# Optimization experiments

Measured on AMD Instinct MI355X. Metric: run time of the kernel, lower is better.

Reference implementation:

```python
import jax, jax.numpy as jnp
import numpy as np

H = 16
N_TASKS, N_DATA, N_DEV = 400_000, 200_000, 8


def _edges(key, n_src, n_dst, e):
    k1, k2 = jax.random.split(key)
    src = jax.random.randint(k1, (e,), 0, n_src)
    dst = jax.random.randint(k2, (e,), 0, n_dst)
    return jnp.stack([src, dst]).astype(jnp.int64)


def setup_inputs() -> dict:
    key = jax.random.key(0)
    ks = jax.random.split(key, 16)
    inp = {
        "x_tasks": jax.random.normal(ks[0], (N_TASKS, 12), jnp.float32),
        "x_data": jax.random.normal(ks[1], (N_DATA, 5), jnp.float32),
        "x_devices": jax.random.normal(ks[2], (N_DEV, 12), jnp.float32),
        "ei_data_tasks": _edges(ks[3], N_DATA, N_TASKS, 1_600_000),
        "ei_tasks_data": _edges(ks[4], N_TASKS, N_DATA, 1_600_000),
        "ei_tasks_devices": _edges(ks[5], N_TASKS, N_DEV, 400_000),
        "ei_devices_tasks": _edges(ks[6], N_DEV, N_TASKS, 400_000),
        "ei_data_devices": _edges(ks[7], N_DATA, N_DEV, 200_000),
        "ei_devices_data": _edges(ks[8], N_DEV, N_DATA, 200_000),
        "ei_tt_to": _edges(ks[9], N_TASKS, N_TASKS, 800_000),
        "ei_tt_from": _edges(ks[10], N_TASKS, N_TASKS, 800_000),
        # stacked GraphConv weights, grouped by input dim
        # W_rel5:  [0]=data->tasks, [1]=data->devices
        "W_rel5": jax.random.normal(ks[11], (2, 5, H), jnp.float32) * 0.3,
        # W_rel12: [0]=tasks->data,[1]=tasks->devices,[2]=devices->tasks,[3]=devices->data,[4]=tt_to,[5]=tt_from
        "W_rel12": jax.random.normal(ks[12], (6, 12, H), jnp.float32) * 0.2,
        # b_rel order: dt_t, t_d, t_dev, dev_t, d_dev, dev_d, tt_to, tt_from
        "b_rel": jax.random.normal(ks[13], (8, H), jnp.float32) * 0.1,
        # W_root5: [0]=tasks->data (dst data), [1]=devices->data
        "W_root5": jax.random.normal(ks[14], (2, 5, H), jnp.float32) * 0.3,
        # W_root12: [0]=data->tasks,[1]=tasks->devices,[2]=devices->tasks,[3]=data->devices,[4]=tt_to,[5]=tt_from
        "W_root12": jax.random.normal(ks[15], (6, 12, H), jnp.float32) * 0.2,
        # LayerNorm params: [0]=tasks, [1]=data, [2]=devices
        "ln_gamma": jnp.ones((3, H), jnp.float32),
        "ln_beta": jnp.zeros((3, H), jnp.float32),
    }
    return inp


def _graph_conv(x_src, x_dst, ei, W_rel, b_rel, W_root):
    # PyG GraphConv(aggr='add'): lin_rel(scatter_add(x_src[src] -> dst)) + lin_root(x_dst)
    agg = jax.ops.segment_sum(x_src[ei[0]], ei[1], num_segments=x_dst.shape[0])
    return agg @ W_rel + b_rel + x_dst @ W_root


def _layer_norm(x, gamma, beta, eps=1e-5):
    mu = jnp.mean(x, axis=-1, keepdims=True)
    var = jnp.mean(jnp.square(x - mu), axis=-1, keepdims=True)
    return (x - mu) * jax.lax.rsqrt(var + eps) * gamma + beta


def reference(x_tasks, x_data, x_devices,
              ei_data_tasks, ei_tasks_data, ei_tasks_devices, ei_devices_tasks,
              ei_data_devices, ei_devices_data, ei_tt_to, ei_tt_from,
              W_rel5, W_rel12, b_rel, W_root5, W_root12, ln_gamma, ln_beta):
    # HeteroConv(aggr='sum'): sum relation outputs per destination node type
    tasks = (
        _graph_conv(x_data, x_tasks, ei_data_tasks, W_rel5[0], b_rel[0], W_root12[0])
        + _graph_conv(x_devices, x_tasks, ei_devices_tasks, W_rel12[2], b_rel[3], W_root12[2])
        + _graph_conv(x_tasks, x_tasks, ei_tt_to, W_rel12[4], b_rel[6], W_root12[4])
        + _graph_conv(x_tasks, x_tasks, ei_tt_from, W_rel12[5], b_rel[7], W_root12[5])
    )
    data = (
        _graph_conv(x_tasks, x_data, ei_tasks_data, W_rel12[0], b_rel[1], W_root5[0])
        + _graph_conv(x_devices, x_data, ei_devices_data, W_rel12[3], b_rel[5], W_root5[1])
    )
    devices = (
        _graph_conv(x_tasks, x_devices, ei_tasks_devices, W_rel12[1], b_rel[2], W_root12[1])
        + _graph_conv(x_data, x_devices, ei_data_devices, W_rel5[1], b_rel[4], W_root12[3])
    )
    slope = 0.01
    tasks = jax.nn.leaky_relu(_layer_norm(tasks, ln_gamma[0], ln_beta[0]), slope)
    data = jax.nn.leaky_relu(_layer_norm(data, ln_gamma[1], ln_beta[1]), slope)
    devices = jax.nn.leaky_relu(_layer_norm(devices, ln_gamma[2], ln_beta[2]), slope)
    return tasks, data, devices
```

## Files before the change

### kernel.cpp

```cpp
#include <hip/hip_runtime.h>
#include <hip/hip_fp16.h>

#define LRELU(v) ((v) >= 0.0f ? (v) : 0.01f * (v))
#define EPB 8192
#define SHIFT 7
#define PAIRS 1600

struct PartDesc {
    const int* src; const int* dst;
    unsigned* part; int* cursor;
    int E, B, cap, chunk0;
};

struct PrepArgs {
    PartDesc r[6];
    int part_end;
    const int *tdev_e; int E_tdev; int sd12_b0, sd12_nb;
    const int *ddev_e; int E_ddev; int sd5_b0, sd5_nb;
    const float *x_tasks, *x_data, *x_dev;
    float *aggT_dev, *aggD_dev;
    __half *h_tasks; int NT; int ct_b0;
    __half *h_data;  int ND; int cd_b0;
};

template<int F>
__device__ __forceinline__ void loadrow(const float* __restrict__ x, unsigned s, float* v) {
    const float* p = x + (size_t)s * F;
    #pragma unroll
    for (int f = 0; f < F; ++f) v[f] = p[f];
}
template<>
__device__ __forceinline__ void loadrow<12>(const float* __restrict__ x, unsigned s, float* v) {
    const float4* p = (const float4*)(x + (size_t)s * 12);
    float4 a = p[0], b = p[1], c = p[2];
    v[0]=a.x; v[1]=a.y; v[2]=a.z; v[3]=a.w;
    v[4]=b.x; v[5]=b.y; v[6]=b.z; v[7]=b.w;
    v[8]=c.x; v[9]=c.y; v[10]=c.z; v[11]=c.w;
}

template<int F>
__device__ void scatter_dev_body(const float* __restrict__ x, const int* __restrict__ src,
                                 const int* __restrict__ dst, int E,
                                 float* __restrict__ agg, float* s_agg,
                                 int bl, int nb, int t)
{
    for (int i = t; i < 8 * F; i += 256) s_agg[i] = 0.0f;
    __syncthreads();
    const int stride = nb * 256;
    for (int e = bl * 256 + t; e < E; e += stride) {
        float v[F];
        loadrow<F>(x, (unsigned)src[e], v);
        int d = dst[e];
        #pragma unroll
        for (int f = 0; f < F; ++f) atomicAdd(&s_agg[d * F + f], v[f]);
    }
    __syncthreads();
    if (t < 8 * F) atomicAdd(&agg[t], s_agg[t]);
}

__global__ __launch_bounds__(256)
void prep_k(PrepArgs A)
{
    __shared__ unsigned shp[2 * PAIRS];
    const int bid = blockIdx.x;
    const int t = threadIdx.x;

    if (bid < A.part_end) {
        unsigned* hist = shp;
        unsigned* base = shp + PAIRS;
        int ri = 0;
        #pragma unroll
        for (int k = 1; k < 6; ++k) if (bid >= A.r[k].chunk0) ri = k;
        const PartDesc d = A.r[ri];
        const int e0 = (bid - d.chunk0) * EPB;
        const int e1 = min(d.E, e0 + EPB);
        const int npair = (d.B + 1) >> 1;

        for (int i = t; i < npair; i += 256) hist[i] = 0u;
        __syncthreads();
        for (int e = e0 + t; e < e1; e += 256) {
            int b = d.dst[e] >> SHIFT;
            atomicAdd(&hist[b >> 1], 1u << ((b & 1) << 4));
        }
        __syncthreads();
        for (int i = t; i < npair; i += 256) {
            unsigned h = hist[i];
            unsigned lo = h & 0xffffu, hi = h >> 16;
            unsigned blo = lo ? (unsigned)atomicAdd(&d.cursor[2 * i],     (int)lo) : 0u;
            unsigned bhi = hi ? (unsigned)atomicAdd(&d.cursor[2 * i + 1], (int)hi) : 0u;
            base[i] = (blo & 0xffffu) | (bhi << 16);
            hist[i] = 0u;
        }
        __syncthreads();
        for (int e = e0 + t; e < e1; e += 256) {
            int dd = d.dst[e];
            int b = dd >> SHIFT;
            unsigned s16 = (unsigned)(b & 1) << 4;
            unsigned r = atomicAdd(&hist[b >> 1], 1u << s16);
            unsigned idx = ((r >> s16) & 0xffffu) + ((base[b >> 1] >> s16) & 0xffffu);
            if ((int)idx < d.cap)
                d.part[(size_t)b * d.cap + idx] =
                    ((unsigned)d.src[e] << SHIFT) | ((unsigned)dd & 127u);
        }
    } else if (bid < A.sd5_b0) {
        scatter_dev_body<12>(A.x_tasks, A.tdev_e, A.tdev_e + A.E_tdev, A.E_tdev,
                             A.aggT_dev, (float*)shp, bid - A.sd12_b0, A.sd12_nb, t);
    } else if (bid < A.ct_b0) {
        scatter_dev_body<5>(A.x_data, A.ddev_e, A.ddev_e + A.E_ddev, A.E_ddev,
                            A.aggD_dev, (float*)shp, bid - A.sd5_b0, A.sd5_nb, t);
    } else if (bid < A.cd_b0) {
        int row = (bid - A.ct_b0) * 256 + t;
        if (row < A.NT) {
            const float* xr = A.x_tasks + (size_t)row * 12;
            __half h[16];
            #pragma unroll
            for (int j = 0; j < 12; ++j) h[j] = __float2half(xr[j]);
            #pragma unroll
            for (int j = 12; j < 16; ++j) h[j] = __half(0.0f);
            uint4* dst = (uint4*)(A.h_tasks + (size_t)row * 16);
            dst[0] = *(const uint4*)h;
            dst[1] = *(const uint4*)(h + 8);
        }
    } else {
        int row = (bid - A.cd_b0) * 256 + t;
        if (row < A.ND) {
            const float* xr = A.x_data + (size_t)row * 5;
            __half h[8];
            #pragma unroll
            for (int j = 0; j < 5; ++j) h[j] = __float2half(xr[j]);
            #pragma unroll
            for (int j = 5; j < 8; ++j) h[j] = __half(0.0f);
            *(uint4*)(A.h_data + (size_t)row * 8) = *(const uint4*)h;
        }
    }
}

struct LoadH8 {
    const __half* x;
    __device__ __forceinline__ void operator()(unsigned s, float* v) const {
        uint4 u = *(const uint4*)(x + (size_t)s * 8);
        const __half2* h = (const __half2*)&u;
        float2 f0 = __half22float2(h[0]);
        float2 f1 = __half22float2(h[1]);
        float2 f2 = __half22float2(h[2]);
        v[0] = f0.x; v[1] = f0.y; v[2] = f1.x; v[3] = f1.y; v[4] = f2.x;
    }
};
struct LoadH16 {
    const __half* x;
    __device__ __forceinline__ void operator()(unsigned s, float* v) const {
        const uint4* p = (const uint4*)(x + (size_t)s * 16);
        uint4 u0 = p[0], u1 = p[1];
        const __half2* a = (const __half2*)&u0;
        const __half2* b = (const __half2*)&u1;
        float2 f;
        f = __half22float2(a[0]); v[0] = f.x; v[1] = f.y;
        f = __half22float2(a[1]); v[2] = f.x; v[3] = f.y;
        f = __half22float2(a[2]); v[4] = f.x; v[5] = f.y;
        f = __half22float2(a[3]); v[6] = f.x; v[7] = f.y;
        f = __half22float2(b[0]); v[8] = f.x; v[9] = f.y;
        f = __half22float2(b[1]); v[10] = f.x; v[11] = f.y;
    }
};
struct LoadF12 {
    const float* x;
    __device__ __forceinline__ void operator()(unsigned s, float* v) const {
        loadrow<12>(x, s, v);
    }
};

template<int F, int STR, class LD>
__device__ __forceinline__
void agg_rel(const unsigned* __restrict__ p, int cnt, LD ld, float* __restrict__ acc, int t)
{
    int i = t;
    for (; i + 256 < cnt; i += 512) {
        unsigned e0 = p[i], e1 = p[i + 256];
        float v0[F], v1[F];
        ld(e0 >> SHIFT, v0);
        ld(e1 >> SHIFT, v1);
        float* a0 = acc + (e0 & 127u) * STR;
        float* a1 = acc + (e1 & 127u) * STR;
        #pragma unroll
        for (int f = 0; f < F; ++f) atomicAdd(a0 + f, v0[f]);
        #pragma unroll
        for (int f = 0; f < F; ++f) atomicAdd(a1 + f, v1[f]);
    }
    if (i < cnt) {
        unsigned e = p[i];
        float v[F];
        ld(e >> SHIFT, v);
        float* a = acc + (e & 127u) * STR;
        #pragma unroll
        for (int f = 0; f < F; ++f) atomicAdd(a + f, v[f]);
    }
}

__device__ __forceinline__ void fma16(float* o, float fj, const float4* __restrict__ w) {
    float4 w0 = w[0], w1 = w[1], w2 = w[2], w3 = w[3];
    o[0] =fmaf(fj,w0.x,o[0]);  o[1] =fmaf(fj,w0.y,o[1]);
    o[2] =fmaf(fj,w0.z,o[2]);  o[3] =fmaf(fj,w0.w,o[3]);
    o[4] =fmaf(fj,w1.x,o[4]);  o[5] =fmaf(fj,w1.y,o[5]);
    o[6] =fmaf(fj,w1.z,o[6]);  o[7] =fmaf(fj,w1.w,o[7]);
    o[8] =fmaf(fj,w2.x,o[8]);  o[9] =fmaf(fj,w2.y,o[9]);
    o[10]=fmaf(fj,w2.z,o[10]); o[11]=fmaf(fj,w2.w,o[11]);
    o[12]=fmaf(fj,w3.x,o[12]); o[13]=fmaf(fj,w3.y,o[13]);
    o[14]=fmaf(fj,w3.z,o[14]); o[15]=fmaf(fj,w3.w,o[15]);
}

__device__ __forceinline__
void ln_store(float* o, const float* __restrict__ sg, const float* __restrict__ sbt,
              float* __restrict__ op)
{
    float mu = 0.0f;
    #pragma unroll
    for (int k = 0; k < 16; ++k) mu += o[k];
    mu *= 0.0625f;
    float var = 0.0f;
    #pragma unroll
    for (int k = 0; k < 16; ++k) { float d = o[k] - mu; var = fmaf(d, d, var); }
    var *= 0.0625f;
    const float r = rsqrtf(var + 1e-5f);
    #pragma unroll
    for (int k = 0; k < 16; ++k) {
        float v = (o[k] - mu) * r * sg[k] + sbt[k];
        o[k] = LRELU(v);
    }
    float4* q = (float4*)op;
    const float4* s = (const float4*)o;
    q[0] = s[0]; q[1] = s[1]; q[2] = s[2]; q[3] = s[3];
}

struct FusedDesc { const unsigned* part; const int* cursor; int cap; };
struct FusedArgs {
    FusedDesc rt[4];
    FusedDesc rd[2];
    const __half *h_tasks, *h_data;
    const float *x_dev, *x_tasks, *x_data;
    const float *aggT_dev, *aggD_dev;
    const float *W_rel5, *W_rel12, *b_rel, *W_root5, *W_root12, *ln_g, *ln_b;
    float *out_tasks, *out_data, *out_dev;
    int NT, ND, NDEV, Bt, Bd;
};

__global__ __launch_bounds__(256, 6)
void fused_k(FusedArgs A)
{
    __shared__ __align__(16) float lds[6144];
    const int bid = blockIdx.x;
    const int t = threadIdx.x;

    if (bid < A.Bt) {
        float* acc = lds;
        float* sW  = lds + 5248;
        float* sb  = lds + 6096;
        float* sg  = lds + 6112;
        float* sbt = lds + 6128;

        for (int i = t; i < 5248; i += 256) acc[i] = 0.0f;
        for (int i = t; i < 80; i += 256) sW[i] = A.W_rel5[i];
        for (int i = t; i < 192; i += 256) {
            sW[80  + i] = A.W_rel12[384 + i];
            sW[272 + i] = A.W_rel12[768 + i];
            sW[464 + i] = A.W_rel12[960 + i];
            sW[656 + i] = A.W_root12[i] + A.W_root12[384 + i]
                        + A.W_root12[768 + i] + A.W_root12[960 + i];
        }
        if (t < 16) {
            sb[t]  = A.b_rel[t] + A.b_rel[48 + t] + A.b_rel[96 + t] + A.b_rel[112 + t];
            sg[t]  = A.ln_g[t];
            sbt[t] = A.ln_b[t];
        }
        __syncthreads();

        const int b = bid;
        { const FusedDesc d = A.rt[0];
          agg_rel<5, 41>(d.part + (size_t)b * d.cap, min(d.cursor[b], d.cap),
                         LoadH8{A.h_data}, acc + 0, t); }
        { const FusedDesc d = A.rt[1];
          agg_rel<12, 41>(d.part + (size_t)b * d.cap, min(d.cursor[b], d.cap),
                          LoadF12{A.x_dev}, acc + 5, t); }
        { const FusedDesc d = A.rt[2];
          agg_rel<12, 41>(d.part + (size_t)b * d.cap, min(d.cursor[b], d.cap),
                          LoadH16{A.h_tasks}, acc + 17, t); }
        { const FusedDesc d = A.rt[3];
          agg_rel<12, 41>(d.part + (size_t)b * d.cap, min(d.cursor[b], d.cap),
                          LoadH16{A.h_tasks}, acc + 29, t); }
        __syncthreads();

        if (t < 128) {
            const int i = (bid << SHIFT) + t;
            if (i < A.NT) {
                const float4* xr = (const float4*)(A.x_tasks + (size_t)i * 12);
                float4 x0 = xr[0], x1 = xr[1], x2 = xr[2];
                float o[16];
                #pragma unroll
                for (int k = 0; k < 16; ++k) o[k] = sb[k];
                const float4* w4 = (const float4*)sW;
                const float* ar = acc + t * 41;
                #pragma unroll
                for (int j = 0; j < 41; ++j) fma16(o, ar[j], w4 + 4 * j);
                float xf[12] = {x0.x,x0.y,x0.z,x0.w, x1.x,x1.y,x1.z,x1.w, x2.x,x2.y,x2.z,x2.w};
                #pragma unroll
                for (int j = 0; j < 12; ++j) fma16(o, xf[j], w4 + 4 * (41 + j));
                ln_store(o, sg, sbt, A.out_tasks + (size_t)i * 16);
            }
        }
    } else if (bid < A.Bt + A.Bd) {
        float* acc = lds;
        float* sW  = lds + 3200;
        float* sb  = lds + 3664;
        float* sg  = lds + 3680;
        float* sbt = lds + 3696;

        for (int i = t; i < 3200; i += 256) acc[i] = 0.0f;
        for (int i = t; i < 192; i += 256) {
            sW[i]       = A.W_rel12[i];
            sW[192 + i] = A.W_rel12[576 + i];
        }
        for (int i = t; i < 80; i += 256)
            sW[384 + i] = A.W_root5[i] + A.W_root5[80 + i];
        if (t < 16) {
            sb[t]  = A.b_rel[16 + t] + A.b_rel[80 + t];
            sg[t]  = A.ln_g[16 + t];
            sbt[t] = A.ln_b[16 + t];
        }
        __syncthreads();

        const int b = bid - A.Bt;
        { const FusedDesc d = A.rd[0];
          agg_rel<12, 25>(d.part + (size_t)b * d.cap, min(d.cursor[b], d.cap),
                          LoadH16{A.h_tasks}, acc + 0, t); }
        { const FusedDesc d = A.rd[1];
          agg_rel<12, 25>(d.part + (size_t)b * d.cap, min(d.cursor[b], d.cap),
                          LoadF12{A.x_dev}, acc + 12, t); }
        __syncthreads();

        if (t < 128) {
            const int i = (b << SHIFT) + t;
            if (i < A.ND) {
                const float* xr = A.x_data + (size_t)i * 5;
                float o[16];
                #pragma unroll
                for (int k = 0; k < 16; ++k) o[k] = sb[k];
                const float4* w4 = (const float4*)sW;
                const float* ar = acc + t * 25;
                #pragma unroll
                for (int j = 0; j < 24; ++j) fma16(o, ar[j], w4 + 4 * j);
                #pragma unroll
                for (int j = 0; j < 5; ++j) fma16(o, xr[j], w4 + 4 * (24 + j));
                ln_store(o, sg, sbt, A.out_data + (size_t)i * 16);
            }
        }
    } else {
        const int i = t;
        if (i < A.NDEV) {
            float o[16];
            #pragma unroll
            for (int k = 0; k < 16; ++k) o[k] = A.b_rel[32 + k] + A.b_rel[64 + k];
            #pragma unroll
            for (int j = 0; j < 12; ++j) {
                float fj = A.aggT_dev[i * 12 + j];
                #pragma unroll
                for (int k = 0; k < 16; ++k) o[k] = fmaf(fj, A.W_rel12[192 + j * 16 + k], o[k]);
            }
            #pragma unroll
            for (int j = 0; j < 5; ++j) {
                float fj = A.aggD_dev[i * 5 + j];
                #pragma unroll
                for (int k = 0; k < 16; ++k) o[k] = fmaf(fj, A.W_rel5[80 + j * 16 + k], o[k]);
            }
            #pragma unroll
            for (int j = 0; j < 12; ++j) {
                float fj = A.x_dev[i * 12 + j];
                #pragma unroll
                for (int k = 0; k < 16; ++k)
                    o[k] = fmaf(fj, A.W_root12[192 + j * 16 + k] + A.W_root12[576 + j * 16 + k], o[k]);
            }
            ln_store(o, A.ln_g + 32, A.ln_b + 32, A.out_dev + (size_t)i * 16);
        }
    }
}

extern "C" void kernel_launch(void* const* d_in, const int* in_sizes, int n_in,
                              void* d_out, int out_size, void* d_ws, size_t ws_size,
                              hipStream_t stream)
{
    const float* x_tasks = (const float*)d_in[0];
    const float* x_data  = (const float*)d_in[1];
    const float* x_dev   = (const float*)d_in[2];
    const int* ei_dt    = (const int*)d_in[3];
    const int* ei_td    = (const int*)d_in[4];
    const int* ei_tdev  = (const int*)d_in[5];
    const int* ei_devt  = (const int*)d_in[6];
    const int* ei_ddev  = (const int*)d_in[7];
    const int* ei_devd  = (const int*)d_in[8];
    const int* ei_to    = (const int*)d_in[9];
    const int* ei_from  = (const int*)d_in[10];
    const float* W_rel5   = (const float*)d_in[11];
    const float* W_rel12  = (const float*)d_in[12];
    const float* b_rel    = (const float*)d_in[13];
    const float* W_root5  = (const float*)d_in[14];
    const float* W_root12 = (const float*)d_in[15];
    const float* ln_g     = (const float*)d_in[16];
    const float* ln_b     = (const float*)d_in[17];

    const int NT   = in_sizes[0] / 12;
    const int ND   = in_sizes[1] / 5;
    const int NDEV = in_sizes[2] / 12;
    const int E_dt   = in_sizes[3]  / 2;
    const int E_td   = in_sizes[4]  / 2;
    const int E_tdev = in_sizes[5]  / 2;
    const int E_devt = in_sizes[6]  / 2;
    const int E_ddev = in_sizes[7]  / 2;
    const int E_devd = in_sizes[8]  / 2;
    const int E_to   = in_sizes[9]  / 2;
    const int E_from = in_sizes[10] / 2;

    const int B_t = (NT + 127) / 128;
    const int B_d = (ND + 127) / 128;

    auto capf = [](int E, int B) {
        int mean = E / B + 1;
        int c = mean + mean / 4 + 128;
        return (c + 3) & ~3;
    };
    const int cap_dt   = capf(E_dt,   B_t);
    const int cap_devt = capf(E_devt, B_t);
    const int cap_to   = capf(E_to,   B_t);
    const int cap_from = capf(E_from, B_t);
    const int cap_td   = capf(E_td,   B_d);
    const int cap_devd = capf(E_devd, B_d);

    float* ws = (float*)d_ws;
    size_t o = 0;
    int* c_dt   = (int*)(ws + o); o += 3200;
    int* c_devt = (int*)(ws + o); o += 3200;
    int* c_to   = (int*)(ws + o); o += 3200;
    int* c_from = (int*)(ws + o); o += 3200;
    int* c_td   = (int*)(ws + o); o += 1600;
    int* c_devd = (int*)(ws + o); o += 1600;
    float* aggT_dev = ws + o; o += 96;
    float* aggD_dev = ws + o; o += 48;
    const size_t zero_bytes = o * sizeof(float);
    o = (o + 3) & ~(size_t)3;
    __half* h_tasks = (__half*)(ws + o); o += (size_t)NT * 8;
    __half* h_data  = (__half*)(ws + o); o += (size_t)ND * 4;
    unsigned* p_dt   = (unsigned*)(ws + o); o += (size_t)B_t * cap_dt;
    unsigned* p_devt = (unsigned*)(ws + o); o += (size_t)B_t * cap_devt;
    unsigned* p_to   = (unsigned*)(ws + o); o += (size_t)B_t * cap_to;
    unsigned* p_from = (unsigned*)(ws + o); o += (size_t)B_t * cap_from;
    unsigned* p_td   = (unsigned*)(ws + o); o += (size_t)B_d * cap_td;
    unsigned* p_devd = (unsigned*)(ws + o); o += (size_t)B_d * cap_devd;

    hipMemsetAsync(d_ws, 0, zero_bytes, stream);

    auto nc = [](int e) { return (e + EPB - 1) / EPB; };
    PrepArgs pa;
    int ch = 0;
    pa.r[0] = { ei_dt,   ei_dt   + E_dt,   p_dt,   c_dt,   E_dt,   B_t, cap_dt,   ch }; ch += nc(E_dt);
    pa.r[1] = { ei_devt, ei_devt + E_devt, p_devt, c_devt, E_devt, B_t, cap_devt, ch }; ch += nc(E_devt);
    pa.r[2] = { ei_to,   ei_to   + E_to,   p_to,   c_to,   E_to,   B_t, cap_to,   ch }; ch += nc(E_to);
    pa.r[3] = { ei_from, ei_from + E_from, p_from, c_from, E_from, B_t, cap_from, ch }; ch += nc(E_from);
    pa.r[4] = { ei_td,   ei_td   + E_td,   p_td,   c_td,   E_td,   B_d, cap_td,   ch }; ch += nc(E_td);
    pa.r[5] = { ei_devd, ei_devd + E_devd, p_devd, c_devd, E_devd, B_d, cap_devd, ch }; ch += nc(E_devd);
    pa.part_end = ch;
    pa.tdev_e = ei_tdev; pa.E_tdev = E_tdev; pa.sd12_b0 = ch; pa.sd12_nb = 192; ch += 192;
    pa.ddev_e = ei_ddev; pa.E_ddev = E_ddev; pa.sd5_b0  = ch; pa.sd5_nb  = 96;  ch += 96;
    pa.x_tasks = x_tasks; pa.x_data = x_data; pa.x_dev = x_dev;
    pa.aggT_dev = aggT_dev; pa.aggD_dev = aggD_dev;
    pa.h_tasks = h_tasks; pa.NT = NT; pa.ct_b0 = ch; ch += (NT + 255) / 256;
    pa.h_data  = h_data;  pa.ND = ND; pa.cd_b0 = ch; ch += (ND + 255) / 256;

    prep_k<<<ch, 256, 0, stream>>>(pa);

    float* out_tasks = (float*)d_out;
    float* out_data  = out_tasks + (size_t)NT * 16;
    float* out_dev   = out_data  + (size_t)ND * 16;

    FusedArgs fa;
    fa.rt[0] = { p_dt,   c_dt,   cap_dt   };
    fa.rt[1] = { p_devt, c_devt, cap_devt };
    fa.rt[2] = { p_to,   c_to,   cap_to   };
    fa.rt[3] = { p_from, c_from, cap_from };
    fa.rd[0] = { p_td,   c_td,   cap_td   };
    fa.rd[1] = { p_devd, c_devd, cap_devd };
    fa.h_tasks = h_tasks; fa.h_data = h_data;
    fa.x_dev = x_dev; fa.x_tasks = x_tasks; fa.x_data = x_data;
    fa.aggT_dev = aggT_dev; fa.aggD_dev = aggD_dev;
    fa.W_rel5 = W_rel5; fa.W_rel12 = W_rel12; fa.b_rel = b_rel;
    fa.W_root5 = W_root5; fa.W_root12 = W_root12; fa.ln_g = ln_g; fa.ln_b = ln_b;
    fa.out_tasks = out_tasks; fa.out_data = out_data; fa.out_dev = out_dev;
    fa.NT = NT; fa.ND = ND; fa.NDEV = NDEV;
    fa.Bt = B_t; fa.Bd = B_d;

    fused_k<<<B_t + B_d + 1, 256, 0, stream>>>(fa);
}
```

Measured before the change: 610.0 us.

## Merge per-relation edge partitions into tagged unified lists and widen fused blocks

Edges from all relations that target the same destination type now go into one shared partition buffer per bucket. Each entry carries a 2-bit relation tag, so the fused kernel walks a single edge list per block and dispatches the gather by tag, instead of running four or two separate aggregation loops. The fused kernel moves from 256 to 512 threads per block. Its linear/LayerNorm epilogue now uses four threads per node, each computing four outputs, with shuffle reductions for the LayerNorm statistics. This is meant to remove per-relation loop tails and idle threads and to raise parallelism in the epilogue. The cost is divergent branching on the tag inside the gather and higher register pressure under the stricter launch bounds.

```diff
diff --git a/kernel.cpp b/kernel.cpp
--- a/kernel.cpp
+++ b/kernel.cpp
@@ -10,6 +10,7 @@
     const int* src; const int* dst;
     unsigned* part; int* cursor;
     int E, B, cap, chunk0;
+    unsigned tag;
 };
 
 struct PrepArgs {
@@ -100,7 +101,7 @@
             unsigned idx = ((r >> s16) & 0xffffu) + ((base[b >> 1] >> s16) & 0xffffu);
             if ((int)idx < d.cap)
                 d.part[(size_t)b * d.cap + idx] =
-                    ((unsigned)d.src[e] << SHIFT) | ((unsigned)dd & 127u);
+                    ((unsigned)d.src[e] << 9) | (((unsigned)dd & 127u) << 2) | d.tag;
         }
     } else if (bid < A.sd5_b0) {
         scatter_dev_body<12>(A.x_tasks, A.tdev_e, A.tdev_e + A.E_tdev, A.E_tdev,
@@ -135,77 +136,81 @@
     }
 }
 
-struct LoadH8 {
-    const __half* x;
-    __device__ __forceinline__ void operator()(unsigned s, float* v) const {
-        uint4 u = *(const uint4*)(x + (size_t)s * 8);
-        const __half2* h = (const __half2*)&u;
-        float2 f0 = __half22float2(h[0]);
-        float2 f1 = __half22float2(h[1]);
-        float2 f2 = __half22float2(h[2]);
-        v[0] = f0.x; v[1] = f0.y; v[2] = f1.x; v[3] = f1.y; v[4] = f2.x;
-    }
+struct FusedArgs {
+    const unsigned *p_task, *p_data;
+    const int *c_task, *c_data;
+    int cap_t, cap_d;
+    const __half *h_tasks, *h_data;
+    const float *x_dev, *x_tasks, *x_data;
+    const float *aggT_dev, *aggD_dev;
+    const float *W_rel5, *W_rel12, *b_rel, *W_root5, *W_root12, *ln_g, *ln_b;
+    float *out_tasks, *out_data, *out_dev;
+    int NT, ND, NDEV, Bt, Bd;
 };
-struct LoadH16 {
-    const __half* x;
-    __device__ __forceinline__ void operator()(unsigned s, float* v) const {
-        const uint4* p = (const uint4*)(x + (size_t)s * 16);
-        uint4 u0 = p[0], u1 = p[1];
-        const __half2* a = (const __half2*)&u0;
-        const __half2* b = (const __half2*)&u1;
-        float2 f;
-        f = __half22float2(a[0]); v[0] = f.x; v[1] = f.y;
-        f = __half22float2(a[1]); v[2] = f.x; v[3] = f.y;
-        f = __half22float2(a[2]); v[4] = f.x; v[5] = f.y;
-        f = __half22float2(a[3]); v[6] = f.x; v[7] = f.y;
-        f = __half22float2(b[0]); v[8] = f.x; v[9] = f.y;
-        f = __half22float2(b[1]); v[10] = f.x; v[11] = f.y;
-    }
-};
-struct LoadF12 {
-    const float* x;
-    __device__ __forceinline__ void operator()(unsigned s, float* v) const {
-        loadrow<12>(x, s, v);
-    }
-};
-
-template<int F, int STR, class LD>
-__device__ __forceinline__
-void agg_rel(const unsigned* __restrict__ p, int cnt, LD ld, float* __restrict__ acc, int t)
-{
-    int i = t;
-    for (; i + 256 < cnt; i += 512) {
-        unsigned e0 = p[i], e1 = p[i + 256];
-        float v0[F], v1[F];
-        ld(e0 >> SHIFT, v0);
-        ld(e1 >> SHIFT, v1);
-        float* a0 = acc + (e0 & 127u) * STR;
-        float* a1 = acc + (e1 & 127u) * STR;
+
+__device__ __forceinline__ void issue_task(unsigned e, const FusedArgs& A, uint4* r) {
+    unsigned rel = e & 3u, s = e >> 9;
+    if (rel == 0u) {
+        r[0] = *(const uint4*)(A.h_data + (size_t)s * 8);
+    } else if (rel == 1u) {
+        const uint4* q = (const uint4*)(A.x_dev + (size_t)s * 12);
+        r[0] = q[0]; r[1] = q[1]; r[2] = q[2];
+    } else {
+        const uint4* q = (const uint4*)(A.h_tasks + (size_t)s * 16);
+        r[0] = q[0]; r[1] = q[1];
+    }
+}
+__device__ __forceinline__ void commit_task(unsigned e, const uint4* r, float* acc) {
+    unsigned rel = e & 3u;
+    float* a = acc + ((e >> 2) & 127u) * 41;
+    if (rel == 0u) {
+        const __half2* h = (const __half2*)r;
+        float2 f0 = __half22float2(h[0]), f1 = __half22float2(h[1]), f2 = __half22float2(h[2]);
+        atomicAdd(a + 0, f0.x); atomicAdd(a + 1, f0.y);
+        atomicAdd(a + 2, f1.x); atomicAdd(a + 3, f1.y);
+        atomicAdd(a + 4, f2.x);
+    } else if (rel == 1u) {
+        const float* f = (const float*)r;
         #pragma unroll
-        for (int f = 0; f < F; ++f) atomicAdd(a0 + f, v0[f]);
+        for (int j = 0; j < 12; ++j) atomicAdd(a + 5 + j, f[j]);
+    } else {
+        float* base = a + (rel == 2u ? 17 : 29);
+        const __half2* h = (const __half2*)r;
         #pragma unroll
-        for (int f = 0; f < F; ++f) atomicAdd(a1 + f, v1[f]);
-    }
-    if (i < cnt) {
-        unsigned e = p[i];
-        float v[F];
-        ld(e >> SHIFT, v);
-        float* a = acc + (e & 127u) * STR;
+        for (int j = 0; j < 6; ++j) {
+            float2 f = __half22float2(h[j]);
+            atomicAdd(base + 2 * j,     f.x);
+            atomicAdd(base + 2 * j + 1, f.y);
+        }
+    }
+}
+
+__device__ __forceinline__ void issue_data(unsigned e, const FusedArgs& A, uint4* r) {
+    unsigned rel = e & 3u, s = e >> 9;
+    if (rel == 0u) {
+        const uint4* q = (const uint4*)(A.h_tasks + (size_t)s * 16);
+        r[0] = q[0]; r[1] = q[1];
+    } else {
+        const uint4* q = (const uint4*)(A.x_dev + (size_t)s * 12);
+        r[0] = q[0]; r[1] = q[1]; r[2] = q[2];
+    }
+}
+__device__ __forceinline__ void commit_data(unsigned e, const uint4* r, float* acc) {
+    unsigned rel = e & 3u;
+    float* a = acc + ((e >> 2) & 127u) * 25;
+    if (rel == 0u) {
+        const __half2* h = (const __half2*)r;
         #pragma unroll
-        for (int f = 0; f < F; ++f) atomicAdd(a + f, v[f]);
-    }
-}
-
-__device__ __forceinline__ void fma16(float* o, float fj, const float4* __restrict__ w) {
-    float4 w0 = w[0], w1 = w[1], w2 = w[2], w3 = w[3];
-    o[0] =fmaf(fj,w0.x,o[0]);  o[1] =fmaf(fj,w0.y,o[1]);
-    o[2] =fmaf(fj,w0.z,o[2]);  o[3] =fmaf(fj,w0.w,o[3]);
-    o[4] =fmaf(fj,w1.x,o[4]);  o[5] =fmaf(fj,w1.y,o[5]);
-    o[6] =fmaf(fj,w1.z,o[6]);  o[7] =fmaf(fj,w1.w,o[7]);
-    o[8] =fmaf(fj,w2.x,o[8]);  o[9] =fmaf(fj,w2.y,o[9]);
-    o[10]=fmaf(fj,w2.z,o[10]); o[11]=fmaf(fj,w2.w,o[11]);
-    o[12]=fmaf(fj,w3.x,o[12]); o[13]=fmaf(fj,w3.y,o[13]);
-    o[14]=fmaf(fj,w3.z,o[14]); o[15]=fmaf(fj,w3.w,o[15]);
+        for (int j = 0; j < 6; ++j) {
+            float2 f = __half22float2(h[j]);
+            atomicAdd(a + 2 * j,     f.x);
+            atomicAdd(a + 2 * j + 1, f.y);
+        }
+    } else {
+        const float* f = (const float*)r;
+        #pragma unroll
+        for (int j = 0; j < 12; ++j) atomicAdd(a + 12 + j, f[j]);
+    }
 }
 
 __device__ __forceinline__
@@ -231,19 +236,7 @@
     q[0] = s[0]; q[1] = s[1]; q[2] = s[2]; q[3] = s[3];
 }
 
-struct FusedDesc { const unsigned* part; const int* cursor; int cap; };
-struct FusedArgs {
-    FusedDesc rt[4];
-    FusedDesc rd[2];
-    const __half *h_tasks, *h_data;
-    const float *x_dev, *x_tasks, *x_data;
-    const float *aggT_dev, *aggD_dev;
-    const float *W_rel5, *W_rel12, *b_rel, *W_root5, *W_root12, *ln_g, *ln_b;
-    float *out_tasks, *out_data, *out_dev;
-    int NT, ND, NDEV, Bt, Bd;
-};
-
-__global__ __launch_bounds__(256, 6)
+__global__ __launch_bounds__(512, 8)
 void fused_k(FusedArgs A)
 {
     __shared__ __align__(16) float lds[6144];
@@ -257,9 +250,9 @@
         float* sg  = lds + 6112;
         float* sbt = lds + 6128;
 
-        for (int i = t; i < 5248; i += 256) acc[i] = 0.0f;
-        for (int i = t; i < 80; i += 256) sW[i] = A.W_rel5[i];
-        for (int i = t; i < 192; i += 256) {
+        for (int i = t; i < 5248; i += 512) acc[i] = 0.0f;
+        for (int i = t; i < 80; i += 512) sW[i] = A.W_rel5[i];
+        for (int i = t; i < 192; i += 512) {
             sW[80  + i] = A.W_rel12[384 + i];
             sW[272 + i] = A.W_rel12[768 + i];
             sW[464 + i] = A.W_rel12[960 + i];
@@ -273,38 +266,59 @@
         }
         __syncthreads();
 
-        const int b = bid;
-        { const FusedDesc d = A.rt[0];
-          agg_rel<5, 41>(d.part + (size_t)b * d.cap, min(d.cursor[b], d.cap),
-                         LoadH8{A.h_data}, acc + 0, t); }
-        { const FusedDesc d = A.rt[1];
-          agg_rel<12, 41>(d.part + (size_t)b * d.cap, min(d.cursor[b], d.cap),
-                          LoadF12{A.x_dev}, acc + 5, t); }
-        { const FusedDesc d = A.rt[2];
-          agg_rel<12, 41>(d.part + (size_t)b * d.cap, min(d.cursor[b], d.cap),
-                          LoadH16{A.h_tasks}, acc + 17, t); }
-        { const FusedDesc d = A.rt[3];
-          agg_rel<12, 41>(d.part + (size_t)b * d.cap, min(d.cursor[b], d.cap),
-                          LoadH16{A.h_tasks}, acc + 29, t); }
-        __syncthreads();
-
-        if (t < 128) {
-            const int i = (bid << SHIFT) + t;
-            if (i < A.NT) {
-                const float4* xr = (const float4*)(A.x_tasks + (size_t)i * 12);
-                float4 x0 = xr[0], x1 = xr[1], x2 = xr[2];
-                float o[16];
-                #pragma unroll
-                for (int k = 0; k < 16; ++k) o[k] = sb[k];
-                const float4* w4 = (const float4*)sW;
-                const float* ar = acc + t * 41;
-                #pragma unroll
-                for (int j = 0; j < 41; ++j) fma16(o, ar[j], w4 + 4 * j);
-                float xf[12] = {x0.x,x0.y,x0.z,x0.w, x1.x,x1.y,x1.z,x1.w, x2.x,x2.y,x2.z,x2.w};
-                #pragma unroll
-                for (int j = 0; j < 12; ++j) fma16(o, xf[j], w4 + 4 * (41 + j));
-                ln_store(o, sg, sbt, A.out_tasks + (size_t)i * 16);
-            }
+        const unsigned* p = A.p_task + (size_t)bid * A.cap_t;
+        const int cnt = min(A.c_task[bid], A.cap_t);
+        int i = t;
+        for (; i + 512 < cnt; i += 1024) {
+            unsigned e0 = p[i], e1 = p[i + 512];
+            uint4 r0[3], r1[3];
+            issue_task(e0, A, r0);
+            issue_task(e1, A, r1);
+            commit_task(e0, r0, acc);
+            commit_task(e1, r1, acc);
+        }
+        if (i < cnt) {
+            unsigned e = p[i];
+            uint4 r[3];
+            issue_task(e, A, r);
+            commit_task(e, r, acc);
+        }
+        __syncthreads();
+
+        const int node = t >> 2, part = t & 3;
+        const int row = (bid << SHIFT) + node;
+        if (row < A.NT) {
+            const float* ar = acc + node * 41;
+            const int p4 = part * 4;
+            float o0 = sb[p4], o1 = sb[p4 + 1], o2 = sb[p4 + 2], o3 = sb[p4 + 3];
+            #pragma unroll
+            for (int f = 0; f < 41; ++f) {
+                float v = ar[f];
+                float4 w = *(const float4*)(sW + f * 16 + p4);
+                o0 = fmaf(v, w.x, o0); o1 = fmaf(v, w.y, o1);
+                o2 = fmaf(v, w.z, o2); o3 = fmaf(v, w.w, o3);
+            }
+            const float* xr = A.x_tasks + (size_t)row * 12;
+            #pragma unroll
+            for (int f = 0; f < 12; ++f) {
+                float v = xr[f];
+                float4 w = *(const float4*)(sW + (41 + f) * 16 + p4);
+                o0 = fmaf(v, w.x, o0); o1 = fmaf(v, w.y, o1);
+                o2 = fmaf(v, w.z, o2); o3 = fmaf(v, w.w, o3);
+            }
+            float s = o0 + o1 + o2 + o3;
+            s += __shfl_xor(s, 1); s += __shfl_xor(s, 2);
+            const float mu = s * 0.0625f;
+            float d0 = o0 - mu, d1 = o1 - mu, d2 = o2 - mu, d3 = o3 - mu;
+            float q = d0*d0 + d1*d1 + d2*d2 + d3*d3;
+            q += __shfl_xor(q, 1); q += __shfl_xor(q, 2);
+            const float r = rsqrtf(q * 0.0625f + 1e-5f);
+            float4 out;
+            out.x = LRELU(d0 * r * sg[p4]     + sbt[p4]);
+            out.y = LRELU(d1 * r * sg[p4 + 1] + sbt[p4 + 1]);
+            out.z = LRELU(d2 * r * sg[p4 + 2] + sbt[p4 + 2]);
+            out.w = LRELU(d3 * r * sg[p4 + 3] + sbt[p4 + 3]);
+            *(float4*)(A.out_tasks + (size_t)row * 16 + p4) = out;
         }
     } else if (bid < A.Bt + A.Bd) {
         float* acc = lds;
@@ -313,12 +327,12 @@
         float* sg  = lds + 3680;
         float* sbt = lds + 3696;
 
-        for (int i = t; i < 3200; i += 256) acc[i] = 0.0f;
-        for (int i = t; i < 192; i += 256) {
+        for (int i = t; i < 3200; i += 512) acc[i] = 0.0f;
+        for (int i = t; i < 192; i += 512) {
             sW[i]       = A.W_rel12[i];
             sW[192 + i] = A.W_rel12[576 + i];
         }
-        for (int i = t; i < 80; i += 256)
+        for (int i = t; i < 80; i += 512)
             sW[384 + i] = A.W_root5[i] + A.W_root5[80 + i];
         if (t < 16) {
             sb[t]  = A.b_rel[16 + t] + A.b_rel[80 + t];
@@ -328,29 +342,59 @@
         __syncthreads();
 
         const int b = bid - A.Bt;
-        { const FusedDesc d = A.rd[0];
-          agg_rel<12, 25>(d.part + (size_t)b * d.cap, min(d.cursor[b], d.cap),
-                          LoadH16{A.h_tasks}, acc + 0, t); }
-        { const FusedDesc d = A.rd[1];
-          agg_rel<12, 25>(d.part + (size_t)b * d.cap, min(d.cursor[b], d.cap),
-                          LoadF12{A.x_dev}, acc + 12, t); }
-        __syncthreads();
-
-        if (t < 128) {
-            const int i = (b << SHIFT) + t;
-            if (i < A.ND) {
-                const float* xr = A.x_data + (size_t)i * 5;
-                float o[16];
-                #pragma unroll
-                for (int k = 0; k < 16; ++k) o[k] = sb[k];
-                const float4* w4 = (const float4*)sW;
-                const float* ar = acc + t * 25;
-                #pragma unroll
-                for (int j = 0; j < 24; ++j) fma16(o, ar[j], w4 + 4 * j);
-                #pragma unroll
-                for (int j = 0; j < 5; ++j) fma16(o, xr[j], w4 + 4 * (24 + j));
-                ln_store(o, sg, sbt, A.out_data + (size_t)i * 16);
-            }
+        const unsigned* p = A.p_data + (size_t)b * A.cap_d;
+        const int cnt = min(A.c_data[b], A.cap_d);
+        int i = t;
+        for (; i + 512 < cnt; i += 1024) {
+            unsigned e0 = p[i], e1 = p[i + 512];
+            uint4 r0[3], r1[3];
+            issue_data(e0, A, r0);
+            issue_data(e1, A, r1);
+            commit_data(e0, r0, acc);
+            commit_data(e1, r1, acc);
+        }
+        if (i < cnt) {
+            unsigned e = p[i];
+            uint4 r[3];
+            issue_data(e, A, r);
+            commit_data(e, r, acc);
+        }
+        __syncthreads();
+
+        const int node = t >> 2, part = t & 3;
+        const int row = (b << SHIFT) + node;
+        if (row < A.ND) {
+            const float* ar = acc + node * 25;
+            const int p4 = part * 4;
+            float o0 = sb[p4], o1 = sb[p4 + 1], o2 = sb[p4 + 2], o3 = sb[p4 + 3];
+            #pragma unroll
+            for (int f = 0; f < 24; ++f) {
+                float v = ar[f];
+                float4 w = *(const float4*)(sW + f * 16 + p4);
+                o0 = fmaf(v, w.x, o0); o1 = fmaf(v, w.y, o1);
+                o2 = fmaf(v, w.z, o2); o3 = fmaf(v, w.w, o3);
+            }
+            const float* xr = A.x_data + (size_t)row * 5;
+            #pragma unroll
+            for (int f = 0; f < 5; ++f) {
+                float v = xr[f];
+                float4 w = *(const float4*)(sW + (24 + f) * 16 + p4);
+                o0 = fmaf(v, w.x, o0); o1 = fmaf(v, w.y, o1);
+                o2 = fmaf(v, w.z, o2); o3 = fmaf(v, w.w, o3);
+            }
+            float s = o0 + o1 + o2 + o3;
+            s += __shfl_xor(s, 1); s += __shfl_xor(s, 2);
+            const float mu = s * 0.0625f;
+            float d0 = o0 - mu, d1 = o1 - mu, d2 = o2 - mu, d3 = o3 - mu;
+            float q = d0*d0 + d1*d1 + d2*d2 + d3*d3;
+            q += __shfl_xor(q, 1); q += __shfl_xor(q, 2);
+            const float r = rsqrtf(q * 0.0625f + 1e-5f);
+            float4 out;
+            out.x = LRELU(d0 * r * sg[p4]     + sbt[p4]);
+            out.y = LRELU(d1 * r * sg[p4 + 1] + sbt[p4 + 1]);
+            out.z = LRELU(d2 * r * sg[p4 + 2] + sbt[p4 + 2]);
+            out.w = LRELU(d3 * r * sg[p4 + 3] + sbt[p4 + 3]);
+            *(float4*)(A.out_data + (size_t)row * 16 + p4) = out;
         }
     } else {
         const int i = t;
@@ -420,50 +464,38 @@
     const int B_t = (NT + 127) / 128;
     const int B_d = (ND + 127) / 128;
 
-    auto capf = [](int E, int B) {
-        int mean = E / B + 1;
+    auto capf = [](long long E, int B) {
+        int mean = (int)(E / B) + 1;
         int c = mean + mean / 4 + 128;
         return (c + 3) & ~3;
     };
-    const int cap_dt   = capf(E_dt,   B_t);
-    const int cap_devt = capf(E_devt, B_t);
-    const int cap_to   = capf(E_to,   B_t);
-    const int cap_from = capf(E_from, B_t);
-    const int cap_td   = capf(E_td,   B_d);
-    const int cap_devd = capf(E_devd, B_d);
+    const int cap_t = capf((long long)E_dt + E_devt + E_to + E_from, B_t);
+    const int cap_d = capf((long long)E_td + E_devd, B_d);
 
     float* ws = (float*)d_ws;
     size_t o = 0;
-    int* c_dt   = (int*)(ws + o); o += 3200;
-    int* c_devt = (int*)(ws + o); o += 3200;
-    int* c_to   = (int*)(ws + o); o += 3200;
-    int* c_from = (int*)(ws + o); o += 3200;
-    int* c_td   = (int*)(ws + o); o += 1600;
-    int* c_devd = (int*)(ws + o); o += 1600;
+    int* c_task = (int*)(ws + o); o += 3200;
+    int* c_data = (int*)(ws + o); o += 1600;
     float* aggT_dev = ws + o; o += 96;
     float* aggD_dev = ws + o; o += 48;
     const size_t zero_bytes = o * sizeof(float);
     o = (o + 3) & ~(size_t)3;
     __half* h_tasks = (__half*)(ws + o); o += (size_t)NT * 8;
     __half* h_data  = (__half*)(ws + o); o += (size_t)ND * 4;
-    unsigned* p_dt   = (unsigned*)(ws + o); o += (size_t)B_t * cap_dt;
-    unsigned* p_devt = (unsigned*)(ws + o); o += (size_t)B_t * cap_devt;
-    unsigned* p_to   = (unsigned*)(ws + o); o += (size_t)B_t * cap_to;
-    unsigned* p_from = (unsigned*)(ws + o); o += (size_t)B_t * cap_from;
-    unsigned* p_td   = (unsigned*)(ws + o); o += (size_t)B_d * cap_td;
-    unsigned* p_devd = (unsigned*)(ws + o); o += (size_t)B_d * cap_devd;
+    unsigned* p_task = (unsigned*)(ws + o); o += (size_t)B_t * cap_t;
+    unsigned* p_data = (unsigned*)(ws + o); o += (size_t)B_d * cap_d;
 
     hipMemsetAsync(d_ws, 0, zero_bytes, stream);
 
     auto nc = [](int e) { return (e + EPB - 1) / EPB; };
     PrepArgs pa;
     int ch = 0;
-    pa.r[0] = { ei_dt,   ei_dt   + E_dt,   p_dt,   c_dt,   E_dt,   B_t, cap_dt,   ch }; ch += nc(E_dt);
-    pa.r[1] = { ei_devt, ei_devt + E_devt, p_devt, c_devt, E_devt, B_t, cap_devt, ch }; ch += nc(E_devt);
-    pa.r[2] = { ei_to,   ei_to   + E_to,   p_to,   c_to,   E_to,   B_t, cap_to,   ch }; ch += nc(E_to);
-    pa.r[3] = { ei_from, ei_from + E_from, p_from, c_from, E_from, B_t, cap_from, ch }; ch += nc(E_from);
-    pa.r[4] = { ei_td,   ei_td   + E_td,   p_td,   c_td,   E_td,   B_d, cap_td,   ch }; ch += nc(E_td);
-    pa.r[5] = { ei_devd, ei_devd + E_devd, p_devd, c_devd, E_devd, B_d, cap_devd, ch }; ch += nc(E_devd);
+    pa.r[0] = { ei_dt,   ei_dt   + E_dt,   p_task, c_task, E_dt,   B_t, cap_t, ch, 0u }; ch += nc(E_dt);
+    pa.r[1] = { ei_devt, ei_devt + E_devt, p_task, c_task, E_devt, B_t, cap_t, ch, 1u }; ch += nc(E_devt);
+    pa.r[2] = { ei_to,   ei_to   + E_to,   p_task, c_task, E_to,   B_t, cap_t, ch, 2u }; ch += nc(E_to);
+    pa.r[3] = { ei_from, ei_from + E_from, p_task, c_task, E_from, B_t, cap_t, ch, 3u }; ch += nc(E_from);
+    pa.r[4] = { ei_td,   ei_td   + E_td,   p_data, c_data, E_td,   B_d, cap_d, ch, 0u }; ch += nc(E_td);
+    pa.r[5] = { ei_devd, ei_devd + E_devd, p_data, c_data, E_devd, B_d, cap_d, ch, 1u }; ch += nc(E_devd);
     pa.part_end = ch;
     pa.tdev_e = ei_tdev; pa.E_tdev = E_tdev; pa.sd12_b0 = ch; pa.sd12_nb = 192; ch += 192;
     pa.ddev_e = ei_ddev; pa.E_ddev = E_ddev; pa.sd5_b0  = ch; pa.sd5_nb  = 96;  ch += 96;
@@ -479,12 +511,9 @@
     float* out_dev   = out_data  + (size_t)ND * 16;
 
     FusedArgs fa;
-    fa.rt[0] = { p_dt,   c_dt,   cap_dt   };
-    fa.rt[1] = { p_devt, c_devt, cap_devt };
-    fa.rt[2] = { p_to,   c_to,   cap_to   };
-    fa.rt[3] = { p_from, c_from, cap_from };
-    fa.rd[0] = { p_td,   c_td,   cap_td   };
-    fa.rd[1] = { p_devd, c_devd, cap_devd };
+    fa.p_task = p_task; fa.p_data = p_data;
+    fa.c_task = c_task; fa.c_data = c_data;
+    fa.cap_t = cap_t; fa.cap_d = cap_d;
     fa.h_tasks = h_tasks; fa.h_data = h_data;
     fa.x_dev = x_dev; fa.x_tasks = x_tasks; fa.x_data = x_data;
     fa.aggT_dev = aggT_dev; fa.aggD_dev = aggD_dev;
@@ -494,5 +523,5 @@
     fa.NT = NT; fa.ND = ND; fa.NDEV = NDEV;
     fa.Bt = B_t; fa.Bd = B_d;
 
-    fused_k<<<B_t + B_d + 1, 256, 0, stream>>>(fa);
-}
+    fused_k<<<B_t + B_d + 1, 512, 0, stream>>>(fa);
+}
```

Result: faster. 597.9 us (-2.0%).
